# Kernel optimization log

Hardware: AMD Instinct MI355X
Metric: run time of the kernel (lower is better)

## Reference

```python
import jax, jax.numpy as jnp
import numpy as np
from jax import lax

N, CI, CO, H, W = 2, 256, 256, 64, 64
K, G, DIL, PAD, STRIDE = 3, 8, 1, 1, 1
P = K * K
CG = CO // G  # group channels = 32


def setup_inputs() -> dict:
    key = jax.random.key(0)
    ks = jax.random.split(key, 24)
    r = lambda i, shape, s=1.0: jax.random.normal(ks[i], shape, jnp.float32) * s
    u = lambda i, shape: jax.random.uniform(ks[i], shape, jnp.float32, 0.5, 1.5)
    return dict(
        x=r(0, (N, CI, H, W)),
        conv1_w=r(1, (CO, CI), CI ** -0.5),
        bn1_g=u(2, (CO,)), bn1_b=r(3, (CO,), 0.1), bn1_m=r(4, (CO,), 0.1), bn1_v=u(5, (CO,)),
        inproj_w=r(6, (CO, CO), CO ** -0.5), inproj_b=r(7, (CO,), 0.02),
        dw_w=r(8, (CO, 1, K, K), 0.2), dw_b=r(9, (CO,), 0.02),
        ln_g=u(10, (CO,)), ln_b=r(11, (CO,), 0.02),
        off_w=r(12, (CO, G * P * 2), CO ** -0.5), off_b=jnp.zeros((G * P * 2,), jnp.float32),
        mask_w=r(13, (CO, G * P), CO ** -0.5), mask_b=jnp.zeros((G * P,), jnp.float32),
        outproj_w=r(14, (CO, CO), CO ** -0.5), outproj_b=r(15, (CO,), 0.02),
        bn2_g=u(16, (CO,)), bn2_b=r(17, (CO,), 0.1), bn2_m=r(18, (CO,), 0.1), bn2_v=u(19, (CO,)),
    )


def _bn(x, g, b, m, v, eps):
    # inference-mode BatchNorm2d on NCHW
    return (x - m[:, None, None]) * (g[:, None, None] * lax.rsqrt(v[:, None, None] + eps)) + b[:, None, None]


def _dcn_core(t, offset, mask):
    # t: (N,H,W,C) projected input; offset: (N,H,W,G*P*2); mask: (N,H,W,G,P) softmaxed
    xp = jnp.pad(t, ((0, 0), (PAD, PAD), (PAD, PAD), (0, 0)))
    H_, W_ = H + 2 * PAD, W + 2 * PAD
    # reference points (sample centers), normalized to padded size
    ry = ((DIL * (K - 1)) / 2 + 0.5 + STRIDE * jnp.arange(H, dtype=t.dtype)) / H_
    rx = ((DIL * (K - 1)) / 2 + 0.5 + STRIDE * jnp.arange(W, dtype=t.dtype)) / W_
    base = (DIL * (K - 1)) // 2
    gx = jnp.linspace(-base, -base + (K - 1) * DIL, K, dtype=t.dtype) / W_
    gy = jnp.linspace(-base, -base + (K - 1) * DIL, K, dtype=t.dtype) / H_
    gxx, gyy = jnp.meshgrid(gx, gy, indexing='ij')  # x varies along axis 0 (torch meshgrid order)
    grid = jnp.stack([gxx, gyy], -1).reshape(P, 2)  # (P,2)
    off = offset.reshape(N, H, W, G, P, 2) / jnp.array([W_, H_], t.dtype)
    loc_x = rx[None, None, :, None, None] + grid[:, 0][None, None, None, None] + off[..., 0]  # (N,H,W,G,P)
    loc_y = ry[None, :, None, None, None] + grid[:, 1][None, None, None, None] + off[..., 1]
    # grid_sample(align_corners=False): pixel = norm*size - 0.5
    px = jnp.transpose(loc_x * W_ - 0.5, (0, 3, 1, 2, 4)).reshape(N, G, H * W * P)
    py = jnp.transpose(loc_y * H_ - 0.5, (0, 3, 1, 2, 4)).reshape(N, G, H * W * P)
    # grouped channels-last image: (N,G,H_*W_,CG)
    xg = jnp.transpose(xp.reshape(N, H_, W_, G, CG), (0, 3, 1, 2, 4)).reshape(N, G, H_ * W_, CG)
    x0 = jnp.floor(px)
    y0 = jnp.floor(py)
    wx1 = px - x0
    wy1 = py - y0
    x0i = x0.astype(jnp.int32)
    y0i = y0.astype(jnp.int32)

    def corner(xi, yi, w):
        valid = (xi >= 0) & (xi <= W_ - 1) & (yi >= 0) & (yi <= H_ - 1)
        idx = jnp.clip(yi, 0, H_ - 1) * W_ + jnp.clip(xi, 0, W_ - 1)
        v = jnp.take_along_axis(xg, idx[..., None], axis=2)  # (N,G,M,CG)
        return v * jnp.where(valid, w, 0.0)[..., None]

    sampled = (corner(x0i, y0i, (1 - wx1) * (1 - wy1))
               + corner(x0i + 1, y0i, wx1 * (1 - wy1))
               + corner(x0i, y0i + 1, (1 - wx1) * wy1)
               + corner(x0i + 1, y0i + 1, wx1 * wy1))
    sampled = sampled.reshape(N, G, H * W, P, CG)
    mg = jnp.transpose(mask, (0, 3, 1, 2, 4)).reshape(N, G, H * W, P)
    out = jnp.einsum('nglpc,nglp->nglc', sampled, mg)
    return jnp.transpose(out, (0, 2, 1, 3)).reshape(N, H, W, G * CG)


def reference(x, conv1_w, bn1_g, bn1_b, bn1_m, bn1_v, inproj_w, inproj_b, dw_w, dw_b,
              ln_g, ln_b, off_w, off_b, mask_w, mask_b, outproj_w, outproj_b,
              bn2_g, bn2_b, bn2_m, bn2_v):
    # Conv(inc, ouc, k=1): 1x1 conv (no bias) + BN(eps=1e-3) + SiLU
    y = jnp.einsum('nchw,oc->nohw', x, conv1_w)
    y = jax.nn.silu(_bn(y, bn1_g, bn1_b, bn1_m, bn1_v, 1e-3))
    t = jnp.transpose(y, (0, 2, 3, 1))  # NHWC
    xproj = t @ inproj_w + inproj_b     # input_proj Linear
    # offset/mask branch: depthwise conv (k=3,s=1,p=1) -> LN over C -> GELU
    z = lax.conv_general_dilated(y, dw_w, (1, 1), ((PAD, PAD), (PAD, PAD)),
                                 feature_group_count=CO,
                                 dimension_numbers=('NCHW', 'OIHW', 'NCHW')) + dw_b[None, :, None, None]
    z = jnp.transpose(z, (0, 2, 3, 1))
    mu = jnp.mean(z, -1, keepdims=True)
    var = jnp.var(z, -1, keepdims=True)
    z = (z - mu) * lax.rsqrt(var + 1e-5) * ln_g + ln_b
    z = jax.nn.gelu(z, approximate=False)
    offset = z @ off_w + off_b  # (N,H,W,G*P*2)
    mask = jax.nn.softmax((z @ mask_w + mask_b).reshape(N, H, W, G, P), axis=-1)
    s = _dcn_core(xproj, offset, mask)
    s = s @ outproj_w + outproj_b  # output_proj Linear
    o = jnp.transpose(s, (0, 3, 1, 2))  # back to NCHW
    return jax.nn.silu(_bn(o, bn2_g, bn2_b, bn2_m, bn2_v, 1e-5))
```

## Files before the change

kernel.cpp:

```cpp
#include <hip/hip_runtime.h>
#include <math.h>

#define CC    256
#define HH    64
#define WW    64
#define HWSZ  4096
#define NPIX  8192
#define MT    16
#define TT    16
#define ASTR  264

typedef __attribute__((ext_vector_type(8))) short short8;
typedef __attribute__((ext_vector_type(4))) float f32x4;

__device__ __forceinline__ float silu_f(float x) { return x / (1.f + __expf(-x)); }

__device__ __forceinline__ short f2bf(float f) {
    unsigned u = __float_as_uint(f);
    unsigned r = (u + 0x7fffu + ((u >> 16) & 1u)) >> 16;
    return (short)r;
}
__device__ __forceinline__ unsigned pk2(float a, float b) {
    return (unsigned)(unsigned short)f2bf(a) | ((unsigned)(unsigned short)f2bf(b) << 16);
}
__device__ __forceinline__ float4 bf4(uint2 u) {
    float4 r;
    r.x = __uint_as_float(u.x << 16);
    r.y = __uint_as_float(u.x & 0xffff0000u);
    r.z = __uint_as_float(u.y << 16);
    r.w = __uint_as_float(u.y & 0xffff0000u);
    return r;
}
__device__ __forceinline__ void bf4acc(uint2 u, float wgt, float* acc) {
    acc[0] += wgt * __uint_as_float(u.x << 16);
    acc[1] += wgt * __uint_as_float(u.x & 0xffff0000u);
    acc[2] += wgt * __uint_as_float(u.y << 16);
    acc[3] += wgt * __uint_as_float(u.y & 0xffff0000u);
}

__global__ void k_prep(const float* __restrict__ cw, const float* __restrict__ ipw,
                       const float* __restrict__ offw, const float* __restrict__ maskw,
                       const float* __restrict__ opw, const float* __restrict__ dww,
                       const float* __restrict__ offb, const float* __restrict__ maskb,
                       const float* __restrict__ g1, const float* __restrict__ b1,
                       const float* __restrict__ m1, const float* __restrict__ v1,
                       const float* __restrict__ g2, const float* __restrict__ b2,
                       const float* __restrict__ m2, const float* __restrict__ v2,
                       short* __restrict__ Wc1b, short* __restrict__ Wipb,
                       short* __restrict__ Whb, short* __restrict__ Wopb,
                       float* __restrict__ dwt,
                       float* __restrict__ bh, float* __restrict__ sc1, float* __restrict__ sh1,
                       float* __restrict__ sc2, float* __restrict__ sh2) {
    int o = blockIdx.x, c = threadIdx.x;
    Wc1b[o * CC + c] = f2bf(cw[o * CC + c]);
    Wipb[o * CC + c] = f2bf(ipw[c * CC + o]);
    float hv = 0.f;
    if (o < 144) hv = offw[c * 144 + o];
    else if (o < 216) hv = maskw[c * 72 + (o - 144)];
    Whb[o * CC + c] = f2bf(hv);
    Wopb[o * CC + c] = f2bf(opw[c * CC + o]);
    if (o < 9) dwt[o * CC + c] = dww[c * 9 + o];
    if (o == 0) {
        float bv = 0.f;
        if (c < 144) bv = offb[c];
        else if (c < 216) bv = maskb[c - 144];
        bh[c] = bv;
        float s1 = g1[c] * rsqrtf(v1[c] + 1e-3f);
        sc1[c] = s1; sh1[c] = b1[c] - m1[c] * s1;
        float s2 = g2[c] * rsqrtf(v2[c] + 1e-5f);
        sc2[c] = s2; sh2[c] = b2[c] - m2[c] * s2;
    }
}

__device__ __forceinline__ void gemm1(const short* As, const short* __restrict__ Wb,
                                      int lane, int n0, f32x4* acc) {
    const int m = lane & 15, q = lane >> 4;
#pragma unroll
    for (int kk = 0; kk < 8; ++kk) {
        int c0 = kk * 32 + q * 8;
        short8 a = *(const short8*)(As + m * ASTR + c0);
        short8 b = *(const short8*)(Wb + (size_t)(n0 + m) * CC + c0);
        *acc = __builtin_amdgcn_mfma_f32_16x16x32_bf16(a, b, *acc, 0, 0, 0);
    }
}

__global__ __launch_bounds__(1024, 8) void k_conv_in(
        const float* __restrict__ x, const short* __restrict__ Wc1b,
        const short* __restrict__ Wipb, const float* __restrict__ sc1,
        const float* __restrict__ sh1, const float* __restrict__ ipb,
        short* __restrict__ ybf, short* __restrict__ xpb) {
    __shared__ __align__(16) short As[MT * ASTR];
    int tid = threadIdx.x, lane = tid & 63, wv = tid >> 6;
    int pix0 = blockIdx.x * MT;
    int n = pix0 >> 12, hw0 = pix0 & (HWSZ - 1);
    int n0 = wv * 16;
    const float* xn = x + (size_t)n * CC * HWSZ;
    {
        int c = tid >> 2, i4 = (tid & 3) * 4;
        float4 v = *(const float4*)(xn + (size_t)c * HWSZ + hw0 + i4);
        As[(i4 + 0) * ASTR + c] = f2bf(v.x);
        As[(i4 + 1) * ASTR + c] = f2bf(v.y);
        As[(i4 + 2) * ASTR + c] = f2bf(v.z);
        As[(i4 + 3) * ASTR + c] = f2bf(v.w);
    }
    __syncthreads();
    f32x4 acc = (f32x4){0.f, 0.f, 0.f, 0.f};
    gemm1(As, Wc1b, lane, n0, &acc);
    __syncthreads();
    int col = lane & 15, qr = (lane >> 4) * 4;
    int o = n0 + col;
    {
        float sc = sc1[o], sh = sh1[o];
#pragma unroll
        for (int r = 0; r < 4; ++r)
            As[(qr + r) * ASTR + o] = f2bf(silu_f(acc[r] * sc + sh));
    }
    __syncthreads();
    *(uint2*)(ybf + (size_t)(pix0 + wv) * CC + lane * 4) =
        *(const uint2*)(As + wv * ASTR + lane * 4);
    acc = (f32x4){0.f, 0.f, 0.f, 0.f};
    gemm1(As, Wipb, lane, n0, &acc);
    {
        float bo = ipb[o];
#pragma unroll
        for (int r = 0; r < 4; ++r)
            xpb[(size_t)(pix0 + qr + r) * CC + o] = f2bf(acc[r] + bo);
    }
}

__global__ __launch_bounds__(1024, 8) void k_tail(
        const short* __restrict__ ybf, const short* __restrict__ xpb,
        const float* __restrict__ dwt, const float* __restrict__ dwb,
        const float* __restrict__ lng, const float* __restrict__ lnb,
        const short* __restrict__ Whb, const float* __restrict__ bh,
        const short* __restrict__ Wopb, const float* __restrict__ opb,
        const float* __restrict__ sc2, const float* __restrict__ sh2,
        float* __restrict__ out) {
    __shared__ __align__(16) short As[TT * ASTR];
    __shared__ __align__(16) float buf[TT * 260];
    float* ml   = buf;
    float* loff = buf + 1216;
    float* xs   = buf;

    int tid = threadIdx.x, lane = tid & 63, wv = tid >> 6;
    int pix0 = blockIdx.x * TT;
    int n = pix0 >> 12, hw0 = pix0 & (HWSZ - 1);
    int h = hw0 >> 6, w0 = hw0 & 63;
    int c0 = lane * 4;
    int n0 = wv * 16;
    int col = lane & 15, qr = (lane >> 4) * 4;

    {
        float4 dwbv = *(const float4*)(dwb + c0);
        float4 lngv = *(const float4*)(lng + c0);
        float4 lnbv = *(const float4*)(lnb + c0);
        const short* yn = ybf + (size_t)n * HWSZ * CC;
        int pix = wv;
        int w = w0 + pix;
        float4 acc = dwbv;
#pragma unroll
        for (int ky = 0; ky < 3; ++ky) {
            int yy = h + ky - 1;
            int yc = min(max(yy, 0), HH - 1);
            float vy = (yy == yc) ? 1.f : 0.f;
#pragma unroll
            for (int kx = 0; kx < 3; ++kx) {
                int xx = w + kx - 1;
                int xc = min(max(xx, 0), WW - 1);
                float vm = vy * ((xx == xc) ? 1.f : 0.f);
                int t = ky * 3 + kx;
                float4 wt = *(const float4*)(dwt + t * CC + c0);
                float4 yv = bf4(*(const uint2*)(yn + (size_t)((yc << 6) + xc) * CC + c0));
                acc.x += yv.x * wt.x * vm;
                acc.y += yv.y * wt.y * vm;
                acc.z += yv.z * wt.z * vm;
                acc.w += yv.w * wt.w * vm;
            }
        }
        float s1 = acc.x + acc.y + acc.z + acc.w;
        float s2 = acc.x * acc.x + acc.y * acc.y + acc.z * acc.z + acc.w * acc.w;
#pragma unroll
        for (int off = 32; off > 0; off >>= 1) {
            s1 += __shfl_xor(s1, off);
            s2 += __shfl_xor(s2, off);
        }
        float mu = s1 * (1.f / 256.f);
        float var = s2 * (1.f / 256.f) - mu * mu;
        float rs = rsqrtf(var + 1e-5f);
        float4 zv;
        zv.x = (acc.x - mu) * rs * lngv.x + lnbv.x;
        zv.y = (acc.y - mu) * rs * lngv.y + lnbv.y;
        zv.z = (acc.z - mu) * rs * lngv.z + lnbv.z;
        zv.w = (acc.w - mu) * rs * lngv.w + lnbv.w;
        zv.x = 0.5f * zv.x * (1.f + erff(zv.x * 0.70710678118654752f));
        zv.y = 0.5f * zv.y * (1.f + erff(zv.y * 0.70710678118654752f));
        zv.z = 0.5f * zv.z * (1.f + erff(zv.z * 0.70710678118654752f));
        zv.w = 0.5f * zv.w * (1.f + erff(zv.w * 0.70710678118654752f));
        *(uint2*)(As + pix * ASTR + c0) = make_uint2(pk2(zv.x, zv.y), pk2(zv.z, zv.w));
    }
    __syncthreads();

    {
        f32x4 acc = (f32x4){0.f, 0.f, 0.f, 0.f};
        gemm1(As, Whb, lane, n0, &acc);
        int o = n0 + col;
        float bo = bh[o];
#pragma unroll
        for (int r = 0; r < 4; ++r) {
            float v = acc[r] + bo;
            int pix = qr + r;
            if (o < 144) loff[pix * 144 + o] = v;
            else if (o < 216) ml[pix * 76 + (o - 144)] = v;
        }
    }
    __syncthreads();

    {
        int g  = lane >> 3;
        int ci = lane & 7;
        int gc0 = g * 32 + ci * 4;
        int pix = wv;
        int w = w0 + pix;
        float e9[9];
        {
            const float* row = ml + pix * 76 + g * 9;
            float mx = -1e30f;
#pragma unroll
            for (int p = 0; p < 9; ++p) { e9[p] = row[p]; mx = fmaxf(mx, e9[p]); }
            float ssum = 0.f;
#pragma unroll
            for (int p = 0; p < 9; ++p) { e9[p] = __expf(e9[p] - mx); ssum += e9[p]; }
            float inv = 1.f / ssum;
#pragma unroll
            for (int p = 0; p < 9; ++p) e9[p] *= inv;
        }
        const float* lp = loff + pix * 144 + g * 18;
        const short* xpn = xpb + (size_t)n * HWSZ * CC;
        float acc4[4];
#pragma unroll
        for (int k = 0; k < 4; ++k) acc4[k] = 0.f;
#pragma unroll
        for (int p = 0; p < 9; ++p) {
            float ox = lp[p * 2], oy = lp[p * 2 + 1];
            float px = (float)(w + p / 3) + ox;
            float py = (float)(h + p % 3) + oy;
            float fx = floorf(px), fy = floorf(py);
            float wx1 = px - fx, wy1 = py - fy;
            int x0 = (int)fx, y0 = (int)fy;
            int x1 = x0 + 1, y1 = y0 + 1;
            int xc0 = min(max(x0, 1), WW), xc1 = min(max(x1, 1), WW);
            int yc0 = min(max(y0, 1), HH), yc1 = min(max(y1, 1), HH);
            float vx0 = (x0 == xc0) ? 1.f : 0.f, vx1 = (x1 == xc1) ? 1.f : 0.f;
            float vy0 = (y0 == yc0) ? 1.f : 0.f, vy1 = (y1 == yc1) ? 1.f : 0.f;
            float mval = e9[p];
            float w00 = (1.f - wx1) * (1.f - wy1) * mval * vx0 * vy0;
            float w10 = wx1 * (1.f - wy1) * mval * vx1 * vy0;
            float w01 = (1.f - wx1) * wy1 * mval * vx0 * vy1;
            float w11 = wx1 * wy1 * mval * vx1 * vy1;
            uint2 u00 = *(const uint2*)(xpn + (size_t)(((yc0 - 1) << 6) + (xc0 - 1)) * CC + gc0);
            uint2 u10 = *(const uint2*)(xpn + (size_t)(((yc0 - 1) << 6) + (xc1 - 1)) * CC + gc0);
            uint2 u01 = *(const uint2*)(xpn + (size_t)(((yc1 - 1) << 6) + (xc0 - 1)) * CC + gc0);
            uint2 u11 = *(const uint2*)(xpn + (size_t)(((yc1 - 1) << 6) + (xc1 - 1)) * CC + gc0);
            bf4acc(u00, w00, acc4);
            bf4acc(u10, w10, acc4);
            bf4acc(u01, w01, acc4);
            bf4acc(u11, w11, acc4);
        }
        *(uint2*)(As + pix * ASTR + gc0) =
            make_uint2(pk2(acc4[0], acc4[1]), pk2(acc4[2], acc4[3]));
    }
    __syncthreads();

    {
        f32x4 acc = (f32x4){0.f, 0.f, 0.f, 0.f};
        gemm1(As, Wopb, lane, n0, &acc);
        int o = n0 + col;
        float bo = opb[o], sc = sc2[o], sh = sh2[o];
#pragma unroll
        for (int r = 0; r < 4; ++r)
            xs[(qr + r) * 260 + o] = silu_f((acc[r] + bo) * sc + sh);
    }
    __syncthreads();

    {
        int i4 = (tid & 3) * 4;
        int o = tid >> 2;
        float* on = out + (size_t)n * CC * HWSZ + hw0 + i4;
        float4 ov;
        ov.x = xs[(i4 + 0) * 260 + o];
        ov.y = xs[(i4 + 1) * 260 + o];
        ov.z = xs[(i4 + 2) * 260 + o];
        ov.w = xs[(i4 + 3) * 260 + o];
        *(float4*)(on + (size_t)o * HWSZ) = ov;
    }
}

extern "C" void kernel_launch(void* const* d_in, const int* in_sizes, int n_in,
                              void* d_out, int out_size, void* d_ws, size_t ws_size,
                              hipStream_t stream) {
    const float* x        = (const float*)d_in[0];
    const float* conv1_w  = (const float*)d_in[1];
    const float* bn1_g    = (const float*)d_in[2];
    const float* bn1_b    = (const float*)d_in[3];
    const float* bn1_m    = (const float*)d_in[4];
    const float* bn1_v    = (const float*)d_in[5];
    const float* inproj_w = (const float*)d_in[6];
    const float* inproj_b = (const float*)d_in[7];
    const float* dw_w     = (const float*)d_in[8];
    const float* dw_b     = (const float*)d_in[9];
    const float* ln_g     = (const float*)d_in[10];
    const float* ln_b     = (const float*)d_in[11];
    const float* off_w    = (const float*)d_in[12];
    const float* off_b    = (const float*)d_in[13];
    const float* mask_w   = (const float*)d_in[14];
    const float* mask_b   = (const float*)d_in[15];
    const float* outproj_w = (const float*)d_in[16];
    const float* outproj_b = (const float*)d_in[17];
    const float* bn2_g    = (const float*)d_in[18];
    const float* bn2_b    = (const float*)d_in[19];
    const float* bn2_m    = (const float*)d_in[20];
    const float* bn2_v    = (const float*)d_in[21];
    float* out = (float*)d_out;

    short* Wc1b = (short*)d_ws;
    short* Wipb = Wc1b + 65536;
    short* Whb  = Wipb + 65536;
    short* Wopb = Whb + 65536;
    float* fp   = (float*)(Wopb + 65536);
    float* dwt  = fp;
    float* bh   = dwt + 9 * CC;
    float* sc1  = bh + 256;
    float* sh1  = sc1 + 256;
    float* sc2  = sh1 + 256;
    float* sh2  = sc2 + 256;
    short* ybf  = (short*)(sh2 + 256);
    short* xpb  = ybf + (size_t)NPIX * CC;

    k_prep<<<dim3(CC), dim3(CC), 0, stream>>>(conv1_w, inproj_w, off_w, mask_w, outproj_w, dw_w,
                                              off_b, mask_b, bn1_g, bn1_b, bn1_m, bn1_v,
                                              bn2_g, bn2_b, bn2_m, bn2_v,
                                              Wc1b, Wipb, Whb, Wopb, dwt, bh, sc1, sh1, sc2, sh2);
    k_conv_in<<<dim3(NPIX / MT), dim3(1024), 0, stream>>>(x, Wc1b, Wipb, sc1, sh1, inproj_b, ybf, xpb);
    k_tail<<<dim3(NPIX / TT), dim3(1024), 0, stream>>>(ybf, xpb, dwt, dw_b, ln_g, ln_b,
                                                       Whb, bh, Wopb, outproj_b, sc2, sh2, out);
}
```

Before: 158.0 us.

## Switch intermediates to fp16, use packed half FMA sampling, coalesce stores, swizzle blocks

Replaces bf16 storage and MFMA with fp16 throughout, which makes conversions cheaper and lets the deformable bilinear sampling accumulate with packed half2 FMAs instead of scalar fp32. The input-projection output is now staged through shared memory so global stores are coalesced rows. The tail kernel's block index is swizzled so that consecutive blocks come from different image regions. The risks are fp16 range and precision loss, since the sampling sums are now accumulated in half precision.

Result: no change. 156.0 us (-1.3%).

```diff
diff --git a/kernel.cpp b/kernel.cpp
--- a/kernel.cpp
+++ b/kernel.cpp
@@ -1,4 +1,5 @@
 #include <hip/hip_runtime.h>
+#include <hip/hip_fp16.h>
 #include <math.h>
 
 #define CC    256
@@ -10,32 +11,25 @@
 #define TT    16
 #define ASTR  264
 
-typedef __attribute__((ext_vector_type(8))) short short8;
+typedef __attribute__((ext_vector_type(8))) _Float16 half8;
 typedef __attribute__((ext_vector_type(4))) float f32x4;
 
 __device__ __forceinline__ float silu_f(float x) { return x / (1.f + __expf(-x)); }
 
-__device__ __forceinline__ short f2bf(float f) {
-    unsigned u = __float_as_uint(f);
-    unsigned r = (u + 0x7fffu + ((u >> 16) & 1u)) >> 16;
-    return (short)r;
-}
-__device__ __forceinline__ unsigned pk2(float a, float b) {
-    return (unsigned)(unsigned short)f2bf(a) | ((unsigned)(unsigned short)f2bf(b) << 16);
-}
-__device__ __forceinline__ float4 bf4(uint2 u) {
-    float4 r;
-    r.x = __uint_as_float(u.x << 16);
-    r.y = __uint_as_float(u.x & 0xffff0000u);
-    r.z = __uint_as_float(u.y << 16);
-    r.w = __uint_as_float(u.y & 0xffff0000u);
-    return r;
-}
-__device__ __forceinline__ void bf4acc(uint2 u, float wgt, float* acc) {
-    acc[0] += wgt * __uint_as_float(u.x << 16);
-    acc[1] += wgt * __uint_as_float(u.x & 0xffff0000u);
-    acc[2] += wgt * __uint_as_float(u.y << 16);
-    acc[3] += wgt * __uint_as_float(u.y & 0xffff0000u);
+__device__ __forceinline__ short f2h(float f) {
+    __half h = __float2half(f);
+    return *reinterpret_cast<short*>(&h);
+}
+__device__ __forceinline__ unsigned h2u(float a, float b) {
+    __half2 h = __floats2half2_rn(a, b);
+    return *reinterpret_cast<unsigned*>(&h);
+}
+__device__ __forceinline__ __half2 u2h(unsigned v) { return *reinterpret_cast<__half2*>(&v); }
+__device__ __forceinline__ unsigned h2raw(__half2 h) { return *reinterpret_cast<unsigned*>(&h); }
+__device__ __forceinline__ float4 h2f4(uint2 u) {
+    float2 a = __half22float2(u2h(u.x));
+    float2 b = __half22float2(u2h(u.y));
+    return make_float4(a.x, a.y, b.x, b.y);
 }
 
 __global__ void k_prep(const float* __restrict__ cw, const float* __restrict__ ipw,
@@ -52,13 +46,13 @@
                        float* __restrict__ bh, float* __restrict__ sc1, float* __restrict__ sh1,
                        float* __restrict__ sc2, float* __restrict__ sh2) {
     int o = blockIdx.x, c = threadIdx.x;
-    Wc1b[o * CC + c] = f2bf(cw[o * CC + c]);
-    Wipb[o * CC + c] = f2bf(ipw[c * CC + o]);
+    Wc1b[o * CC + c] = f2h(cw[o * CC + c]);
+    Wipb[o * CC + c] = f2h(ipw[c * CC + o]);
     float hv = 0.f;
     if (o < 144) hv = offw[c * 144 + o];
     else if (o < 216) hv = maskw[c * 72 + (o - 144)];
-    Whb[o * CC + c] = f2bf(hv);
-    Wopb[o * CC + c] = f2bf(opw[c * CC + o]);
+    Whb[o * CC + c] = f2h(hv);
+    Wopb[o * CC + c] = f2h(opw[c * CC + o]);
     if (o < 9) dwt[o * CC + c] = dww[c * 9 + o];
     if (o == 0) {
         float bv = 0.f;
@@ -78,9 +72,9 @@
 #pragma unroll
     for (int kk = 0; kk < 8; ++kk) {
         int c0 = kk * 32 + q * 8;
-        short8 a = *(const short8*)(As + m * ASTR + c0);
-        short8 b = *(const short8*)(Wb + (size_t)(n0 + m) * CC + c0);
-        *acc = __builtin_amdgcn_mfma_f32_16x16x32_bf16(a, b, *acc, 0, 0, 0);
+        half8 a = *(const half8*)(As + m * ASTR + c0);
+        half8 b = *(const half8*)(Wb + (size_t)(n0 + m) * CC + c0);
+        *acc = __builtin_amdgcn_mfma_f32_16x16x32_f16(a, b, *acc, 0, 0, 0);
     }
 }
 
@@ -98,10 +92,10 @@
     {
         int c = tid >> 2, i4 = (tid & 3) * 4;
         float4 v = *(const float4*)(xn + (size_t)c * HWSZ + hw0 + i4);
-        As[(i4 + 0) * ASTR + c] = f2bf(v.x);
-        As[(i4 + 1) * ASTR + c] = f2bf(v.y);
-        As[(i4 + 2) * ASTR + c] = f2bf(v.z);
-        As[(i4 + 3) * ASTR + c] = f2bf(v.w);
+        As[(i4 + 0) * ASTR + c] = f2h(v.x);
+        As[(i4 + 1) * ASTR + c] = f2h(v.y);
+        As[(i4 + 2) * ASTR + c] = f2h(v.z);
+        As[(i4 + 3) * ASTR + c] = f2h(v.w);
     }
     __syncthreads();
     f32x4 acc = (f32x4){0.f, 0.f, 0.f, 0.f};
@@ -113,19 +107,23 @@
         float sc = sc1[o], sh = sh1[o];
 #pragma unroll
         for (int r = 0; r < 4; ++r)
-            As[(qr + r) * ASTR + o] = f2bf(silu_f(acc[r] * sc + sh));
+            As[(qr + r) * ASTR + o] = f2h(silu_f(acc[r] * sc + sh));
     }
     __syncthreads();
     *(uint2*)(ybf + (size_t)(pix0 + wv) * CC + lane * 4) =
         *(const uint2*)(As + wv * ASTR + lane * 4);
     acc = (f32x4){0.f, 0.f, 0.f, 0.f};
     gemm1(As, Wipb, lane, n0, &acc);
+    __syncthreads();
     {
         float bo = ipb[o];
 #pragma unroll
         for (int r = 0; r < 4; ++r)
-            xpb[(size_t)(pix0 + qr + r) * CC + o] = f2bf(acc[r] + bo);
-    }
+            As[(qr + r) * ASTR + o] = f2h(acc[r] + bo);
+    }
+    __syncthreads();
+    *(uint2*)(xpb + (size_t)(pix0 + wv) * CC + lane * 4) =
+        *(const uint2*)(As + wv * ASTR + lane * 4);
 }
 
 __global__ __launch_bounds__(1024, 8) void k_tail(
@@ -143,7 +141,9 @@
     float* xs   = buf;
 
     int tid = threadIdx.x, lane = tid & 63, wv = tid >> 6;
-    int pix0 = blockIdx.x * TT;
+    int bid = blockIdx.x;
+    int swz = ((bid & 7) << 6) | (bid >> 3);
+    int pix0 = swz * TT;
     int n = pix0 >> 12, hw0 = pix0 & (HWSZ - 1);
     int h = hw0 >> 6, w0 = hw0 & 63;
     int c0 = lane * 4;
@@ -170,7 +170,7 @@
                 float vm = vy * ((xx == xc) ? 1.f : 0.f);
                 int t = ky * 3 + kx;
                 float4 wt = *(const float4*)(dwt + t * CC + c0);
-                float4 yv = bf4(*(const uint2*)(yn + (size_t)((yc << 6) + xc) * CC + c0));
+                float4 yv = h2f4(*(const uint2*)(yn + (size_t)((yc << 6) + xc) * CC + c0));
                 acc.x += yv.x * wt.x * vm;
                 acc.y += yv.y * wt.y * vm;
                 acc.z += yv.z * wt.z * vm;
@@ -196,7 +196,7 @@
         zv.y = 0.5f * zv.y * (1.f + erff(zv.y * 0.70710678118654752f));
         zv.z = 0.5f * zv.z * (1.f + erff(zv.z * 0.70710678118654752f));
         zv.w = 0.5f * zv.w * (1.f + erff(zv.w * 0.70710678118654752f));
-        *(uint2*)(As + pix * ASTR + c0) = make_uint2(pk2(zv.x, zv.y), pk2(zv.z, zv.w));
+        *(uint2*)(As + pix * ASTR + c0) = make_uint2(h2u(zv.x, zv.y), h2u(zv.z, zv.w));
     }
     __syncthreads();
 
@@ -236,9 +236,7 @@
         }
         const float* lp = loff + pix * 144 + g * 18;
         const short* xpn = xpb + (size_t)n * HWSZ * CC;
-        float acc4[4];
-#pragma unroll
-        for (int k = 0; k < 4; ++k) acc4[k] = 0.f;
+        __half2 a01 = u2h(0u), a23 = u2h(0u);
 #pragma unroll
         for (int p = 0; p < 9; ++p) {
             float ox = lp[p * 2], oy = lp[p * 2 + 1];
@@ -261,13 +259,16 @@
             uint2 u10 = *(const uint2*)(xpn + (size_t)(((yc0 - 1) << 6) + (xc1 - 1)) * CC + gc0);
             uint2 u01 = *(const uint2*)(xpn + (size_t)(((yc1 - 1) << 6) + (xc0 - 1)) * CC + gc0);
             uint2 u11 = *(const uint2*)(xpn + (size_t)(((yc1 - 1) << 6) + (xc1 - 1)) * CC + gc0);
-            bf4acc(u00, w00, acc4);
-            bf4acc(u10, w10, acc4);
-            bf4acc(u01, w01, acc4);
-            bf4acc(u11, w11, acc4);
-        }
-        *(uint2*)(As + pix * ASTR + gc0) =
-            make_uint2(pk2(acc4[0], acc4[1]), pk2(acc4[2], acc4[3]));
+            __half2 W00 = __float2half2_rn(w00);
+            __half2 W10 = __float2half2_rn(w10);
+            __half2 W01 = __float2half2_rn(w01);
+            __half2 W11 = __float2half2_rn(w11);
+            a01 = __hfma2(u2h(u00.x), W00, a01); a23 = __hfma2(u2h(u00.y), W00, a23);
+            a01 = __hfma2(u2h(u10.x), W10, a01); a23 = __hfma2(u2h(u10.y), W10, a23);
+            a01 = __hfma2(u2h(u01.x), W01, a01); a23 = __hfma2(u2h(u01.y), W01, a23);
+            a01 = __hfma2(u2h(u11.x), W11, a01); a23 = __hfma2(u2h(u11.y), W11, a23);
+        }
+        *(uint2*)(As + pix * ASTR + gc0) = make_uint2(h2raw(a01), h2raw(a23));
     }
     __syncthreads();
 
```
